# Kernel optimization log

Measured on AMD Instinct MI355X. Metric: run time of the kernel, lower is better.

## Reference

```python
import jax, jax.numpy as jnp
import numpy as np


def setup_inputs() -> dict:
    key = jax.random.key(0)
    k1, k2 = jax.random.split(key)
    B, C, H, W = 8, 64, 128, 128
    C_w, ks = 8, 3
    x = jax.random.normal(k1, (B, C, H, W), dtype=jnp.float32)
    w = jax.random.normal(k2, (B, C_w, ks * ks, H, W), dtype=jnp.float32)
    return {"x": x, "w": w}


def _ska_2d(x, w):
    # x: (B,C,H,W); w: (B,C_w,ks^2,H,W); groups = C // C_w
    B, C, H, W = x.shape
    C_w, ks2 = w.shape[1], w.shape[2]
    ks = int(round(np.sqrt(ks2)))
    pad = ks // 2
    groups = C // C_w
    x_pad = jnp.pad(x, ((0, 0), (0, 0), (pad, pad), (pad, pad)))
    # Gather shifted views instead of materializing a giant unfold copy; order
    # matches F.unfold (kernel row-major: i outer, j inner).
    patches = jnp.stack(
        [x_pad[:, :, i:i + H, j:j + W] for i in range(ks) for j in range(ks)],
        axis=2,
    )  # (B, C, ks^2, H, W)
    # Split channels as (groups, C_w): output channel c = g*C_w + cw uses weight channel cw.
    p = patches.reshape(B, groups, C_w, ks2, H, W)
    out = jnp.einsum('bgckhw,bckhw->bgchw', p, w)  # sum over kernel positions k
    return out.reshape(B, C, H, W)


def reference(x, w):
    return _ska_2d(x, w)
```

## Files before the change

kernel.cpp:

```cpp
#include <hip/hip_runtime.h>
#include <stdint.h>


#define SKA_W 128
#define SKA_HW (128 * 128)
#define TILE_ROWS 8
#define STAGE_ROWS 10

typedef float vf4 __attribute__((ext_vector_type(4)));

__global__ __launch_bounds__(256, 4) void SKA_44830868635847_kernel(
        const float* __restrict__ x,
        const float* __restrict__ wgt,
        float* __restrict__ out) {
    __shared__ float lds[8 * STAGE_ROWS * SKA_W];

    const int t     = threadIdx.x;
    const int bid   = blockIdx.x;
    const int htile = bid & 15;
    const int cw    = (bid >> 4) & 7;
    const int b     = bid >> 7;
    const int h0    = htile * TILE_ROWS;

    const int w4 = t & 31;
    const int hl = t >> 5;
    const int h  = h0 + hl;
    const int w0 = w4 * 4;

    const float* xb = x + (size_t)(b * 64 + cw) * SKA_HW;
    const int wavebase = t & ~63;
#pragma unroll
    for (int rep = 0; rep < 10; ++rep) {
        int idx = rep * 256 + t;
        int ch  = idx / 320;
        int rem = idx - ch * 320;
        int r   = rem >> 5;
        int c4  = rem & 31;
        int xrow = h0 - 1 + r;
        xrow = xrow < 0 ? 0 : (xrow > 127 ? 127 : xrow);
        const float* gsrc = xb + (size_t)ch * 8 * SKA_HW + (size_t)xrow * SKA_W + c4 * 4;
        __builtin_amdgcn_global_load_lds(
            (const __attribute__((address_space(1))) uint32_t*)gsrc,
            (__attribute__((address_space(3))) uint32_t*)&lds[(size_t)(rep * 256 + wavebase) * 4],
            16, 0, 0);
    }

    const float* wbase = wgt + ((size_t)(b * 8 + cw) * 9) * SKA_HW + (size_t)h * SKA_W + w0;
    vf4 wv[9];
#pragma unroll
    for (int k = 0; k < 9; ++k)
        wv[k] = *(const vf4*)(wbase + (size_t)k * SKA_HW);
    if (h == 0)   { wv[0] = (vf4)(0.f); wv[1] = (vf4)(0.f); wv[2] = (vf4)(0.f); }
    if (h == 127) { wv[6] = (vf4)(0.f); wv[7] = (vf4)(0.f); wv[8] = (vf4)(0.f); }

    __syncthreads();

    const size_t obase = (size_t)(b * 64 + cw) * SKA_HW + (size_t)h * SKA_W + w0;
#pragma unroll
    for (int g = 0; g < 8; ++g) {
        vf4 acc = (vf4)(0.f);
#pragma unroll
        for (int i = 0; i < 3; ++i) {
            const float* lrow = &lds[(g * STAGE_ROWS + hl + i) * SKA_W + w0];
            vf4 mid = *(const vf4*)lrow;
            float xl  = __shfl_up(mid.w, 1);
            xl  = (w4 == 0)  ? 0.f : xl;
            float xr4 = __shfl_down(mid.x, 1);
            xr4 = (w4 == 31) ? 0.f : xr4;
            vf4 wl = wv[i * 3 + 0];
            vf4 wm = wv[i * 3 + 1];
            vf4 wr = wv[i * 3 + 2];
            acc.x += wl.x * xl    + wm.x * mid.x + wr.x * mid.y;
            acc.y += wl.y * mid.x + wm.y * mid.y + wr.y * mid.z;
            acc.z += wl.z * mid.y + wm.z * mid.z + wr.z * mid.w;
            acc.w += wl.w * mid.z + wm.w * mid.w + wr.w * xr4;
        }
        *(vf4*)(out + obase + (size_t)g * 8 * SKA_HW) = acc;
    }
}

extern "C" void kernel_launch(void* const* d_in, const int* in_sizes, int n_in,
                              void* d_out, int out_size, void* d_ws, size_t ws_size,
                              hipStream_t stream) {
    const float* x   = (const float*)d_in[0];
    const float* wgt = (const float*)d_in[1];
    float* out = (float*)d_out;

    SKA_44830868635847_kernel<<<1024, 256, 0, stream>>>(x, wgt, out);
}
```

Before: 102.7 us.

## Shrink row tile to 4 and fetch halo rows directly from global memory

Halves the row tile to 4 rows per block with 128 threads and 2048 blocks, and stages only the tile's own rows in LDS. The two halo rows are no longer staged; edge-row threads read them straight from global memory per group. The goal is a smaller LDS footprint and more blocks for occupancy and load balance. The cost is a larger halo fraction (now read as divergent global loads by edge threads only) and per-block overhead, since each thread still loads all 9 weight vectors.

```diff
diff --git a/kernel.cpp b/kernel.cpp
--- a/kernel.cpp
+++ b/kernel.cpp
@@ -4,22 +4,21 @@
 
 #define SKA_W 128
 #define SKA_HW (128 * 128)
-#define TILE_ROWS 8
-#define STAGE_ROWS 10
+#define TILE_ROWS 4
 
 typedef float vf4 __attribute__((ext_vector_type(4)));
 
-__global__ __launch_bounds__(256, 4) void SKA_44830868635847_kernel(
+__global__ __launch_bounds__(128, 4) void SKA_44830868635847_kernel(
         const float* __restrict__ x,
         const float* __restrict__ wgt,
         float* __restrict__ out) {
-    __shared__ float lds[8 * STAGE_ROWS * SKA_W];
+    __shared__ float lds[8 * TILE_ROWS * SKA_W];
 
     const int t     = threadIdx.x;
     const int bid   = blockIdx.x;
-    const int htile = bid & 15;
-    const int cw    = (bid >> 4) & 7;
-    const int b     = bid >> 7;
+    const int htile = bid & 31;
+    const int cw    = (bid >> 5) & 7;
+    const int b     = bid >> 8;
     const int h0    = htile * TILE_ROWS;
 
     const int w4 = t & 31;
@@ -30,18 +29,14 @@
     const float* xb = x + (size_t)(b * 64 + cw) * SKA_HW;
     const int wavebase = t & ~63;
 #pragma unroll
-    for (int rep = 0; rep < 10; ++rep) {
-        int idx = rep * 256 + t;
-        int ch  = idx / 320;
-        int rem = idx - ch * 320;
-        int r   = rem >> 5;
-        int c4  = rem & 31;
-        int xrow = h0 - 1 + r;
-        xrow = xrow < 0 ? 0 : (xrow > 127 ? 127 : xrow);
-        const float* gsrc = xb + (size_t)ch * 8 * SKA_HW + (size_t)xrow * SKA_W + c4 * 4;
+    for (int rep = 0; rep < 8; ++rep) {
+        int idx = rep * 128 + t;
+        int ch  = idx >> 7;
+        int rem = idx & 127;
+        const float* gsrc = xb + (size_t)ch * 8 * SKA_HW + (size_t)h0 * SKA_W + rem * 4;
         __builtin_amdgcn_global_load_lds(
             (const __attribute__((address_space(1))) uint32_t*)gsrc,
-            (__attribute__((address_space(3))) uint32_t*)&lds[(size_t)(rep * 256 + wavebase) * 4],
+            (__attribute__((address_space(3))) uint32_t*)&lds[(size_t)(rep * 128 + wavebase) * 4],
             16, 0, 0);
     }
 
@@ -53,16 +48,33 @@
     if (h == 0)   { wv[0] = (vf4)(0.f); wv[1] = (vf4)(0.f); wv[2] = (vf4)(0.f); }
     if (h == 127) { wv[6] = (vf4)(0.f); wv[7] = (vf4)(0.f); wv[8] = (vf4)(0.f); }
 
+    const bool is_top = (hl == 0), is_bot = (hl == TILE_ROWS - 1);
+    int xrow_extra = is_top ? (h0 - 1 < 0 ? 0 : h0 - 1)
+                            : (h0 + TILE_ROWS > 127 ? 127 : h0 + TILE_ROWS);
+
     __syncthreads();
 
     const size_t obase = (size_t)(b * 64 + cw) * SKA_HW + (size_t)h * SKA_W + w0;
+    const int hu = (hl - 1 < 0) ? 0 : hl - 1;
+    const int hd = (hl + 1 > TILE_ROWS - 1) ? TILE_ROWS - 1 : hl + 1;
 #pragma unroll
     for (int g = 0; g < 8; ++g) {
+        vf4 extra = (vf4)(0.f);
+        if (is_top || is_bot)
+            extra = *(const vf4*)(xb + (size_t)g * 8 * SKA_HW + (size_t)xrow_extra * SKA_W + w0);
+
+        const float* lbase = &lds[g * TILE_ROWS * SKA_W];
+        vf4 m_up  = *(const vf4*)(lbase + hu * SKA_W + w0);
+        vf4 m_mid = *(const vf4*)(lbase + hl * SKA_W + w0);
+        vf4 m_dn  = *(const vf4*)(lbase + hd * SKA_W + w0);
+        vf4 r0 = is_top ? extra : m_up;
+        vf4 r2 = is_bot ? extra : m_dn;
+        vf4 rows[3] = {r0, m_mid, r2};
+
         vf4 acc = (vf4)(0.f);
 #pragma unroll
         for (int i = 0; i < 3; ++i) {
-            const float* lrow = &lds[(g * STAGE_ROWS + hl + i) * SKA_W + w0];
-            vf4 mid = *(const vf4*)lrow;
+            vf4 mid = rows[i];
             float xl  = __shfl_up(mid.w, 1);
             xl  = (w4 == 0)  ? 0.f : xl;
             float xr4 = __shfl_down(mid.x, 1);
@@ -86,5 +98,5 @@
     const float* wgt = (const float*)d_in[1];
     float* out = (float*)d_out;
 
-    SKA_44830868635847_kernel<<<1024, 256, 0, stream>>>(x, wgt, out);
+    SKA_44830868635847_kernel<<<2048, 128, 0, stream>>>(x, wgt, out);
 }
```

Result: slower. 106.4 us (+3.6%).
